# Performance work log

Measured on AMD Instinct MI355X. Metric: run time of the kernel, lower is better.

Reference implementation:

```python
import jax, jax.numpy as jnp
import numpy as np

B, C_IN, C_OUT, N, K = 1, 64, 64, 50000, 20


def setup_inputs() -> dict:
    key = jax.random.key(0)
    k1, k2, k3, k4, k5 = jax.random.split(key, 5)
    x = jax.random.normal(k1, (B, C_IN, N, 1), dtype=jnp.float32)
    edge_index = jax.random.randint(k2, (2, B, N, K), 0, N, dtype=jnp.int64)
    dis = jax.random.uniform(k3, (B, N, K), dtype=jnp.float32)
    W = jax.random.normal(k4, (C_OUT, 2 * C_IN), dtype=jnp.float32) * (2.0 / (2 * C_IN)) ** 0.5
    b = jnp.zeros((C_OUT,), dtype=jnp.float32)
    att_w = jax.random.normal(k5, (K,), dtype=jnp.float32) * (2.0 / K) ** 0.5
    att_b = jnp.zeros((1,), dtype=jnp.float32)
    return {"x": x, "edge_index": edge_index, "dis": dis, "W": W, "b": b,
            "att_w": att_w, "att_b": att_b}


def reference(x, edge_index, dis, W, b, att_w, att_b):
    # x: [B, C, N, 1]; edge_index: [2, B, N, K]; dis: [B, N, K]
    x2 = x[..., 0]  # [B, C, N]
    gather = jax.vmap(lambda xb, ib: xb[:, ib])  # per-batch: [C,N] idx[N,K] -> [C,N,K]
    x_i = gather(x2, edge_index[1])  # [B, C, N, K]
    x_j = gather(x2, edge_index[0])  # [B, C, N, K]
    feat = jnp.concatenate([x_i, x_j - x_i], axis=1)  # [B, 2C, N, K]
    # 1x1 conv == channel contraction
    feat = jax.nn.relu(jnp.einsum('oc,bcnk->bonk', W, feat) + b[None, :, None, None])
    # attention over the k channel of dis -> per-node scaler
    scaler = jnp.tanh(jnp.einsum('k,bnk->bn', att_w, dis) + att_b) + 1.0  # [B, N]
    suppression = 2.0 * jax.nn.sigmoid(-dis * scaler[:, :, None])  # [B, N, K]
    feat = feat * suppression[:, None, :, :]  # [B, C_out, N, K]
    return jnp.max(feat, axis=-1, keepdims=True)  # [B, C_out, N, 1]
```

## Files before the change

kernel.cpp:

```cpp
#include <hip/hip_runtime.h>
#include <hip/hip_bf16.h>

#define NN 50000
#define CC 64
#define KK 20

static __device__ __forceinline__ ushort f2bf(float f) {
    unsigned int u = __float_as_uint(f);
    unsigned int r = (u + 0x7FFFu + ((u >> 16) & 1u)) >> 16;
    return (ushort)r;
}
static __device__ __forceinline__ float bfl(unsigned int u) {
    return __uint_as_float(u << 16);
}
static __device__ __forceinline__ float bfh(unsigned int u) {
    return __uint_as_float(u & 0xffff0000u);
}

__global__ __launch_bounds__(256) void prep_kernel(
    const float* __restrict__ x,
    const float* __restrict__ W,
    const float* __restrict__ b,
    ushort* __restrict__ yA,
    ushort* __restrict__ yB)
{
    __shared__ float At[64][66];
    __shared__ float Bt[64][66];
    __shared__ float xt[64][132];

    const int t = threadIdx.x;
    for (int i = t; i < 64 * 64; i += 256) {
        int c = i >> 6, ci = i & 63;
        float w1 = W[c * 128 + ci];
        float w2 = W[c * 128 + 64 + ci];
        At[ci][c] = w1 - w2;
        Bt[ci][c] = w2;
    }

    const int n0 = blockIdx.x * 128;
    {
        const int q  = t & 31;
        const int cb = t >> 5;
        const float4* x4 = (const float4*)x;
        const int nq = (n0 >> 2) + q;
        #pragma unroll
        for (int i = 0; i < 8; i++) {
            const int ci = cb * 8 + i;
            float4 v = (nq < 12500) ? x4[ci * 12500 + nq]
                                    : float4{0.f, 0.f, 0.f, 0.f};
            *(float4*)&xt[ci][q * 4] = v;
        }
    }
    __syncthreads();

    const int c2 = t & 31;
    const int g  = t >> 5;

    float aA0[16], aA1[16], aB0[16], aB1[16];
    #pragma unroll
    for (int j = 0; j < 16; j++) { aA0[j]=0.f; aA1[j]=0.f; aB0[j]=0.f; aB1[j]=0.f; }

    for (int ci = 0; ci < 64; ci++) {
        const float2 a  = *(const float2*)&At[ci][c2 * 2];
        const float2 w2 = *(const float2*)&Bt[ci][c2 * 2];
        const float4* xr = (const float4*)&xt[ci][g * 16];
        #pragma unroll
        for (int q = 0; q < 4; q++) {
            float4 xv = xr[q];
            aA0[q*4+0] += a.x*xv.x;  aA1[q*4+0] += a.y*xv.x;
            aB0[q*4+0] += w2.x*xv.x; aB1[q*4+0] += w2.y*xv.x;
            aA0[q*4+1] += a.x*xv.y;  aA1[q*4+1] += a.y*xv.y;
            aB0[q*4+1] += w2.x*xv.y; aB1[q*4+1] += w2.y*xv.y;
            aA0[q*4+2] += a.x*xv.z;  aA1[q*4+2] += a.y*xv.z;
            aB0[q*4+2] += w2.x*xv.z; aB1[q*4+2] += w2.y*xv.z;
            aA0[q*4+3] += a.x*xv.w;  aA1[q*4+3] += a.y*xv.w;
            aB0[q*4+3] += w2.x*xv.w; aB1[q*4+3] += w2.y*xv.w;
        }
    }

    const float b0 = b[c2 * 2], b1 = b[c2 * 2 + 1];
    unsigned int* yA32 = (unsigned int*)yA;
    unsigned int* yB32 = (unsigned int*)yB;
    #pragma unroll
    for (int j = 0; j < 16; j++) {
        const int n = n0 + g * 16 + j;
        if (n < NN) {
            yA32[n * 32 + c2] = (unsigned int)f2bf(aA0[j] + b0)
                              | ((unsigned int)f2bf(aA1[j] + b1) << 16);
            yB32[n * 32 + c2] = (unsigned int)f2bf(aB0[j])
                              | ((unsigned int)f2bf(aB1[j]) << 16);
        }
    }
}

__global__ __launch_bounds__(256) void edge_kernel(
    const ushort* __restrict__ yA,
    const ushort* __restrict__ yB,
    const int* __restrict__ ej,
    const int* __restrict__ ei,
    const float* __restrict__ dis,
    const float* __restrict__ att_w,
    const float* __restrict__ att_b,
    float* __restrict__ out)
{
    __shared__ float tile[16][68];

    const int t    = threadIdx.x;
    const int lane = t & 63;
    const int w    = t >> 6;
    const int g    = lane >> 4;
    const int l    = lane & 15;
    const int n0   = blockIdx.x * 16;
    const int nb   = n0 + w * 4;

    const float aw = (lane < KK) ? att_w[lane] : 0.f;
    const float ab = att_b[0];

    float d4[4]; int ii4[4], jj4[4];
    #pragma unroll
    for (int s = 0; s < 4; s++) {
        const int n = nb + s;
        float d = 0.f; int ii = 0, jj = 0;
        if (lane < KK) {
            d  = dis[n * KK + lane];
            ii = ei[n * KK + lane];
            jj = ej[n * KK + lane];
        }
        d4[s] = d; ii4[s] = ii; jj4[s] = jj;
    }

    float sup4[4];
    #pragma unroll
    for (int s = 0; s < 4; s++) {
        float p = aw * d4[s];
        #pragma unroll
        for (int off = 16; off > 0; off >>= 1) p += __shfl_down(p, off);
        const float scaler = tanhf(__shfl(p, 0) + ab) + 1.0f;
        sup4[s] = 2.0f / (1.0f + __expf(d4[s] * scaler));
    }

    const uint2* A2 = (const uint2*)yA;
    const uint2* B2 = (const uint2*)yB;

    #pragma unroll
    for (int s = 0; s < 4; s++) {
        float4 m = {0.f, 0.f, 0.f, 0.f};
        #pragma unroll
        for (int kb = 0; kb < 5; kb++) {
            const int   src = kb * 4 + g;
            const int   i_k = __shfl(ii4[s], src);
            const int   j_k = __shfl(jj4[s], src);
            const float sp  = __shfl(sup4[s], src);
            const uint2 a  = A2[(size_t)i_k * 16 + l];
            const uint2 bb = B2[(size_t)j_k * 16 + l];
            float v;
            v = fmaxf(bfl(a.x) + bfl(bb.x), 0.f) * sp;  m.x = fmaxf(m.x, v);
            v = fmaxf(bfh(a.x) + bfh(bb.x), 0.f) * sp;  m.y = fmaxf(m.y, v);
            v = fmaxf(bfl(a.y) + bfl(bb.y), 0.f) * sp;  m.z = fmaxf(m.z, v);
            v = fmaxf(bfh(a.y) + bfh(bb.y), 0.f) * sp;  m.w = fmaxf(m.w, v);
        }
        #pragma unroll
        for (int mask = 16; mask <= 32; mask <<= 1) {
            m.x = fmaxf(m.x, __shfl_xor(m.x, mask));
            m.y = fmaxf(m.y, __shfl_xor(m.y, mask));
            m.z = fmaxf(m.z, __shfl_xor(m.z, mask));
            m.w = fmaxf(m.w, __shfl_xor(m.w, mask));
        }
        if (g == 0) *(float4*)&tile[w * 4 + s][l * 4] = m;
    }
    __syncthreads();

    #pragma unroll
    for (int it = 0; it < 4; it++) {
        const int c  = it * 16 + (t >> 4);
        const int nl = t & 15;
        out[(size_t)c * NN + n0 + nl] = tile[nl][c];
    }
}

extern "C" void kernel_launch(void* const* d_in, const int* in_sizes, int n_in,
                              void* d_out, int out_size, void* d_ws, size_t ws_size,
                              hipStream_t stream) {
    const float* x     = (const float*)d_in[0];
    const int*   e     = (const int*)d_in[1];
    const float* dis   = (const float*)d_in[2];
    const float* W     = (const float*)d_in[3];
    const float* b     = (const float*)d_in[4];
    const float* att_w = (const float*)d_in[5];
    const float* att_b = (const float*)d_in[6];
    float* out = (float*)d_out;

    ushort* yA = (ushort*)d_ws;
    ushort* yB = yA + (size_t)NN * 64;

    prep_kernel<<<(NN + 127) / 128, 256, 0, stream>>>(x, W, b, yA, yB);
    edge_kernel<<<NN / 16, 256, 0, stream>>>(yA, yB, e, e + NN * KK, dis,
                                             att_w, att_b, out);
}
```

Before: 126.3 us.

## Split gathered features into channel halves and precompute suppression in prep kernel

The bf16 feature tables are reorganised into two channel-half pools, and the edge kernel grid is doubled so each block gathers only 32 channels from one half. The aim is a smaller random-gather working set per pass, so it stays better in cache. The suppression weights (attention scaler, tanh rewritten via exp, then sigmoid) are now computed once in the prep kernel and stored to a global buffer, which removes the per-edge dis loads and shuffle reductions from the edge kernel. Nontemporal loads and stores are added for the edge indices and the output. In exchange, the edge indices and suppression values are read twice, once per half, and the prep kernel does extra work.

```diff
diff --git a/kernel.cpp b/kernel.cpp
--- a/kernel.cpp
+++ b/kernel.cpp
@@ -1,9 +1,10 @@
 #include <hip/hip_runtime.h>
-#include <hip/hip_bf16.h>
 
 #define NN 50000
-#define CC 64
 #define KK 20
+
+__device__ __align__(256) ushort g_pool[2][2][NN * 32];
+__device__ __align__(256) float  g_sup[NN * KK];
 
 static __device__ __forceinline__ ushort f2bf(float f) {
     unsigned int u = __float_as_uint(f);
@@ -21,14 +22,19 @@
     const float* __restrict__ x,
     const float* __restrict__ W,
     const float* __restrict__ b,
-    ushort* __restrict__ yA,
-    ushort* __restrict__ yB)
+    const float* __restrict__ dis,
+    const float* __restrict__ att_w,
+    const float* __restrict__ att_b)
 {
     __shared__ float At[64][66];
     __shared__ float Bt[64][66];
     __shared__ float xt[64][132];
-
-    const int t = threadIdx.x;
+    __shared__ float disL[128 * KK];
+    __shared__ float scalerL[128];
+
+    const int t  = threadIdx.x;
+    const int n0 = blockIdx.x * 128;
+
     for (int i = t; i < 64 * 64; i += 256) {
         int c = i >> 6, ci = i & 63;
         float w1 = W[c * 128 + ci];
@@ -36,8 +42,6 @@
         At[ci][c] = w1 - w2;
         Bt[ci][c] = w2;
     }
-
-    const int n0 = blockIdx.x * 128;
     {
         const int q  = t & 31;
         const int cb = t >> 5;
@@ -51,7 +55,25 @@
             *(float4*)&xt[ci][q * 4] = v;
         }
     }
+    for (int i = t; i < 128 * KK; i += 256) {
+        const int gi = n0 * KK + i;
+        disL[i] = (gi < NN * KK) ? dis[gi] : 0.f;
+    }
     __syncthreads();
+
+    if (t < 128) {
+        float z = att_b[0];
+        #pragma unroll
+        for (int k = 0; k < KK; k++) z += att_w[k] * disL[t * KK + k];
+        scalerL[t] = 2.f / (1.f + __expf(-2.f * z));
+    }
+    __syncthreads();
+
+    for (int i = t; i < 128 * KK; i += 256) {
+        const int gi = n0 * KK + i;
+        if (gi < NN * KK)
+            g_sup[gi] = 2.f / (1.f + __expf(disL[i] * scalerL[i / KK]));
+    }
 
     const int c2 = t & 31;
     const int g  = t >> 5;
@@ -79,80 +101,69 @@
     }
 
     const float b0 = b[c2 * 2], b1 = b[c2 * 2 + 1];
-    unsigned int* yA32 = (unsigned int*)yA;
-    unsigned int* yB32 = (unsigned int*)yB;
+    const int h  = c2 >> 4;
+    const int pp = c2 & 15;
+    unsigned int* pool32 = (unsigned int*)g_pool;
+    const size_t baseA = (size_t)(h * 2 + 0) * NN * 16;
+    const size_t baseB = (size_t)(h * 2 + 1) * NN * 16;
     #pragma unroll
     for (int j = 0; j < 16; j++) {
         const int n = n0 + g * 16 + j;
         if (n < NN) {
-            yA32[n * 32 + c2] = (unsigned int)f2bf(aA0[j] + b0)
-                              | ((unsigned int)f2bf(aA1[j] + b1) << 16);
-            yB32[n * 32 + c2] = (unsigned int)f2bf(aB0[j])
-                              | ((unsigned int)f2bf(aB1[j]) << 16);
+            pool32[baseA + (size_t)n * 16 + pp] =
+                (unsigned int)f2bf(aA0[j] + b0) | ((unsigned int)f2bf(aA1[j] + b1) << 16);
+            pool32[baseB + (size_t)n * 16 + pp] =
+                (unsigned int)f2bf(aB0[j]) | ((unsigned int)f2bf(aB1[j]) << 16);
         }
     }
 }
 
 __global__ __launch_bounds__(256) void edge_kernel(
-    const ushort* __restrict__ yA,
-    const ushort* __restrict__ yB,
     const int* __restrict__ ej,
     const int* __restrict__ ei,
-    const float* __restrict__ dis,
-    const float* __restrict__ att_w,
-    const float* __restrict__ att_b,
     float* __restrict__ out)
 {
-    __shared__ float tile[16][68];
+    __shared__ float tile[16][36];
 
     const int t    = threadIdx.x;
     const int lane = t & 63;
     const int w    = t >> 6;
-    const int g    = lane >> 4;
-    const int l    = lane & 15;
-    const int n0   = blockIdx.x * 16;
+    const int g    = lane >> 3;
+    const int q    = lane & 7;
+    const int bx   = blockIdx.x;
+    const int h    = (bx >= 3125) ? 1 : 0;
+    const int n0   = (bx - h * 3125) * 16;
     const int nb   = n0 + w * 4;
 
-    const float aw = (lane < KK) ? att_w[lane] : 0.f;
-    const float ab = att_b[0];
-
-    float d4[4]; int ii4[4], jj4[4];
+    const char* pA = (const char*)&g_pool[h][0][0];
+    const char* pB = (const char*)&g_pool[h][1][0];
+
+    int offI[4], offJ[4]; float sup4[4];
     #pragma unroll
     for (int s = 0; s < 4; s++) {
         const int n = nb + s;
-        float d = 0.f; int ii = 0, jj = 0;
+        int ii = 0, jj = 0; float sp = 0.f;
         if (lane < KK) {
-            d  = dis[n * KK + lane];
-            ii = ei[n * KK + lane];
-            jj = ej[n * KK + lane];
-        }
-        d4[s] = d; ii4[s] = ii; jj4[s] = jj;
-    }
-
-    float sup4[4];
-    #pragma unroll
-    for (int s = 0; s < 4; s++) {
-        float p = aw * d4[s];
-        #pragma unroll
-        for (int off = 16; off > 0; off >>= 1) p += __shfl_down(p, off);
-        const float scaler = tanhf(__shfl(p, 0) + ab) + 1.0f;
-        sup4[s] = 2.0f / (1.0f + __expf(d4[s] * scaler));
-    }
-
-    const uint2* A2 = (const uint2*)yA;
-    const uint2* B2 = (const uint2*)yB;
+            ii = __builtin_nontemporal_load(&ei[n * KK + lane]);
+            jj = __builtin_nontemporal_load(&ej[n * KK + lane]);
+            sp = __builtin_nontemporal_load(&g_sup[n * KK + lane]);
+        }
+        offI[s] = ii << 6;
+        offJ[s] = jj << 6;
+        sup4[s] = sp;
+    }
 
     #pragma unroll
     for (int s = 0; s < 4; s++) {
         float4 m = {0.f, 0.f, 0.f, 0.f};
         #pragma unroll
-        for (int kb = 0; kb < 5; kb++) {
-            const int   src = kb * 4 + g;
-            const int   i_k = __shfl(ii4[s], src);
-            const int   j_k = __shfl(jj4[s], src);
+        for (int r = 0; r < 3; r++) {
+            const int   src = r * 8 + g;
+            const int   oi  = __shfl(offI[s], src);
+            const int   oj  = __shfl(offJ[s], src);
             const float sp  = __shfl(sup4[s], src);
-            const uint2 a  = A2[(size_t)i_k * 16 + l];
-            const uint2 bb = B2[(size_t)j_k * 16 + l];
+            const uint2 a   = *(const uint2*)(pA + oi + q * 8);
+            const uint2 bb  = *(const uint2*)(pB + oj + q * 8);
             float v;
             v = fmaxf(bfl(a.x) + bfl(bb.x), 0.f) * sp;  m.x = fmaxf(m.x, v);
             v = fmaxf(bfh(a.x) + bfh(bb.x), 0.f) * sp;  m.y = fmaxf(m.y, v);
@@ -160,21 +171,22 @@
             v = fmaxf(bfh(a.y) + bfh(bb.y), 0.f) * sp;  m.w = fmaxf(m.w, v);
         }
         #pragma unroll
-        for (int mask = 16; mask <= 32; mask <<= 1) {
+        for (int mask = 8; mask <= 32; mask <<= 1) {
             m.x = fmaxf(m.x, __shfl_xor(m.x, mask));
             m.y = fmaxf(m.y, __shfl_xor(m.y, mask));
             m.z = fmaxf(m.z, __shfl_xor(m.z, mask));
             m.w = fmaxf(m.w, __shfl_xor(m.w, mask));
         }
-        if (g == 0) *(float4*)&tile[w * 4 + s][l * 4] = m;
+        if (g == 0) *(float4*)&tile[w * 4 + s][q * 4] = m;
     }
     __syncthreads();
 
     #pragma unroll
-    for (int it = 0; it < 4; it++) {
+    for (int it = 0; it < 2; it++) {
         const int c  = it * 16 + (t >> 4);
         const int nl = t & 15;
-        out[(size_t)c * NN + n0 + nl] = tile[nl][c];
+        __builtin_nontemporal_store(tile[nl][c],
+                                    &out[(size_t)(h * 32 + c) * NN + n0 + nl]);
     }
 }
 
@@ -190,10 +202,8 @@
     const float* att_b = (const float*)d_in[6];
     float* out = (float*)d_out;
 
-    ushort* yA = (ushort*)d_ws;
-    ushort* yB = yA + (size_t)NN * 64;
-
-    prep_kernel<<<(NN + 127) / 128, 256, 0, stream>>>(x, W, b, yA, yB);
-    edge_kernel<<<NN / 16, 256, 0, stream>>>(yA, yB, e, e + NN * KK, dis,
-                                             att_w, att_b, out);
-}
+    (void)d_ws; (void)ws_size;
+
+    prep_kernel<<<(NN + 127) / 128, 256, 0, stream>>>(x, W, b, dis, att_w, att_b);
+    edge_kernel<<<2 * 3125, 256, 0, stream>>>(e, e + NN * KK, out);
+}
```

New measurement: 144.6 us. 14.5% more time.
